# Performance work log

Hardware: AMD Instinct MI355X
Metric: run time of the kernel (lower is better)

The kernel has to match this reference:

```python
import jax, jax.numpy as jnp
import numpy as np

S, B, H = 512, 256, 500


def setup_inputs() -> dict:
    key = jax.random.key(0)
    k1, k2, k3, k4, k5 = jax.random.split(key, 5)
    return {
        "hidden": jax.random.normal(k1, (1, B, H), dtype=jnp.float32),
        "encoder_output": jax.random.normal(k2, (S, B, H), dtype=jnp.float32),
        "W_attn": jax.random.normal(k3, (H, 2 * H), dtype=jnp.float32) * 0.02,
        "b_attn": jax.random.normal(k4, (H,), dtype=jnp.float32) * 0.02,
        "v": jax.random.normal(k5, (H,), dtype=jnp.float32),
    }


def reference(hidden, encoder_output, W_attn, b_attn, v):
    # hidden: [1, B, H] -> broadcast to [S, B, H]; concat -> [S, B, 2H]
    s, b, h = encoder_output.shape
    h_exp = jnp.broadcast_to(hidden, (s, b, h))
    cat = jnp.concatenate([h_exp, encoder_output], axis=2)  # [S, B, 2H]
    # Linear(2H -> H) with torch convention W: [out, in], then tanh
    energy = jnp.tanh(jnp.einsum("sbi,hi->sbh", cat, W_attn) + b_attn)  # [S, B, H]
    scores = jnp.einsum("sbh,h->sb", energy, v)  # [S, B]
    attn = jax.nn.softmax(scores.T, axis=1)  # [B, S]
    return attn[:, None, :]  # [B, 1, S]
```

## Files before the change

kernel.cpp:

```cpp
#include <hip/hip_runtime.h>
#include <hip/hip_fp16.h>

#define S_DIM 512
#define B_DIM 256
#define H_DIM 500
#define HP    512
#define M_DIM (S_DIM * B_DIM)

typedef _Float16 half8_t __attribute__((ext_vector_type(8)));
typedef float    f32x4  __attribute__((ext_vector_type(4)));

#define WS_W2H 0
#define WS_A   (512 * 1024)
#define WS_VP  (1024 * 1024)
#define WS_SC  (1024 * 1024 + 4096)

__global__ void prep_w2_v(const float* __restrict__ W, const float* __restrict__ v,
                          _Float16* __restrict__ W2h, float* __restrict__ vp) {
    int idx = blockIdx.x * blockDim.x + threadIdx.x;
#pragma unroll
    for (int r = 0; r < 2; ++r) {
        int e = idx + r * 131072;
        int h = e >> 9, k = e & 511;
        float val = (h < H_DIM && k < H_DIM) ? W[h * 1000 + 500 + k] : 0.0f;
        W2h[e] = (_Float16)val;
    }
    if (idx < HP) vp[idx] = (idx < H_DIM) ? v[idx] : 0.0f;
}

__global__ void prep_A(const float* __restrict__ hidden, const float* __restrict__ W,
                       const float* __restrict__ b_attn, float* __restrict__ A) {
    int b = blockIdx.x;
    int t = threadIdx.x;
    __shared__ float hs[HP];
    hs[t] = (t < H_DIM) ? hidden[b * H_DIM + t] : 0.0f;
    __syncthreads();
    float acc = 0.0f;
    if (t < H_DIM) {
        acc = b_attn[t];
        const float4* wr = (const float4*)(W + t * 1000);
        const float4* hr = (const float4*)hs;
#pragma unroll 5
        for (int i = 0; i < 125; ++i) {
            float4 w4 = wr[i], h4 = hr[i];
            acc += w4.x * h4.x + w4.y * h4.y + w4.z * h4.z + w4.w * h4.w;
        }
    }
    A[b * HP + t] = acc;
}

__launch_bounds__(512, 2)
__global__ void fused_attn_gemm(const float* __restrict__ enc,
                                const _Float16* __restrict__ W2h,
                                const float* __restrict__ Aws,
                                const float* __restrict__ vp,
                                float* __restrict__ scores_t) {
    __shared__ _Float16 As[2][128][32];
    __shared__ _Float16 Bs[2][HP][32];
    __shared__ float    red[4][128];

    const int tid  = threadIdx.x;
    const int lane = tid & 63;
    const int wid  = tid >> 6;
    const int wm   = wid >> 2;
    const int wn   = wid & 3;
    const int l15  = lane & 15;
    const int lq   = lane >> 4;
    const int m0   = blockIdx.x * 128;

    const int srow = tid >> 2;
    const int sc0  = (tid & 3) * 8;

    f32x4 acc[4][8];
#pragma unroll
    for (int a = 0; a < 4; ++a)
#pragma unroll
        for (int b = 0; b < 8; ++b) acc[a][b] = 0;

    auto stage = [&](int buf, int kk) {
        {
            const float* g = enc + (size_t)(m0 + srow) * H_DIM;
            half8_t hv;
            if (kk + sc0 + 8 <= H_DIM) {
                float4 f0 = *(const float4*)(g + kk + sc0);
                float4 f1 = *(const float4*)(g + kk + sc0 + 4);
                hv[0] = (_Float16)f0.x; hv[1] = (_Float16)f0.y;
                hv[2] = (_Float16)f0.z; hv[3] = (_Float16)f0.w;
                hv[4] = (_Float16)f1.x; hv[5] = (_Float16)f1.y;
                hv[6] = (_Float16)f1.z; hv[7] = (_Float16)f1.w;
            } else {
#pragma unroll
                for (int u = 0; u < 8; ++u) {
                    int k = kk + sc0 + u;
                    hv[u] = (k < H_DIM) ? (_Float16)g[k] : (_Float16)0.0f;
                }
            }
            *(half8_t*)&As[buf][srow][sc0] = hv;
        }
#pragma unroll
        for (int r = 0; r < 4; ++r) {
            int row = srow + r * 128;
            half8_t hv = *(const half8_t*)(W2h + row * HP + kk + sc0);
            *(half8_t*)&Bs[buf][row][sc0] = hv;
        }
    };

    stage(0, 0);
#pragma unroll 2
    for (int ks = 0; ks < 16; ++ks) {
        int cur = ks & 1;
        __syncthreads();
        if (ks + 1 < 16) stage(cur ^ 1, (ks + 1) * 32);

        half8_t af[4], bf[8];
#pragma unroll
        for (int mf = 0; mf < 4; ++mf)
            af[mf] = *(const half8_t*)&As[cur][wm * 64 + mf * 16 + l15][lq * 8];
#pragma unroll
        for (int nf = 0; nf < 8; ++nf)
            bf[nf] = *(const half8_t*)&Bs[cur][wn * 128 + nf * 16 + l15][lq * 8];
#pragma unroll
        for (int mf = 0; mf < 4; ++mf)
#pragma unroll
            for (int nf = 0; nf < 8; ++nf)
                acc[mf][nf] = __builtin_amdgcn_mfma_f32_16x16x32_f16(af[mf], bf[nf], acc[mf][nf], 0, 0, 0);
    }

    float vpv[8];
#pragma unroll
    for (int nf = 0; nf < 8; ++nf) vpv[nf] = vp[wn * 128 + nf * 16 + l15];

    const int bloc  = (blockIdx.x & 1) * 128 + wm * 64;
    const int s_idx = blockIdx.x >> 1;

#pragma unroll
    for (int mf = 0; mf < 4; ++mf) {
        float pj[4] = {0, 0, 0, 0};
#pragma unroll
        for (int nf = 0; nf < 8; ++nf) {
            int h = wn * 128 + nf * 16 + l15;
#pragma unroll
            for (int j = 0; j < 4; ++j) {
                int b = bloc + mf * 16 + lq * 4 + j;
                float x = acc[mf][nf][j] + Aws[b * HP + h];
                float xc = fminf(fmaxf(x, -9.0f), 9.0f);
                float e  = __expf(2.0f * xc);
                float th = (e - 1.0f) / (e + 1.0f);
                pj[j] += vpv[nf] * th;
            }
        }
#pragma unroll
        for (int j = 0; j < 4; ++j) {
            float s = pj[j];
            s += __shfl_xor(s, 1); s += __shfl_xor(s, 2);
            s += __shfl_xor(s, 4); s += __shfl_xor(s, 8);
            if (l15 == 0) red[wn][wm * 64 + mf * 16 + lq * 4 + j] = s;
        }
    }
    __syncthreads();
    if (tid < 128) {
        float sc = red[0][tid] + red[1][tid] + red[2][tid] + red[3][tid];
        int b = (blockIdx.x & 1) * 128 + tid;
        scores_t[b * S_DIM + s_idx] = sc;
    }
}

__global__ void softmax_rows(const float* __restrict__ scores_t, float* __restrict__ out) {
    int b = blockIdx.x;
    int t = threadIdx.x;
    int lane = t & 63, wid = t >> 6;
    float v0 = scores_t[b * S_DIM + t];
    float v1 = scores_t[b * S_DIM + t + 256];
    float m = fmaxf(v0, v1);
#pragma unroll
    for (int off = 1; off < 64; off <<= 1) m = fmaxf(m, __shfl_xor(m, off));
    __shared__ float sm[4], ss[4];
    if (lane == 0) sm[wid] = m;
    __syncthreads();
    m = fmaxf(fmaxf(sm[0], sm[1]), fmaxf(sm[2], sm[3]));
    float e0 = __expf(v0 - m), e1 = __expf(v1 - m);
    float sum = e0 + e1;
#pragma unroll
    for (int off = 1; off < 64; off <<= 1) sum += __shfl_xor(sum, off);
    if (lane == 0) ss[wid] = sum;
    __syncthreads();
    sum = ss[0] + ss[1] + ss[2] + ss[3];
    float inv = 1.0f / sum;
    out[b * S_DIM + t]       = e0 * inv;
    out[b * S_DIM + t + 256] = e1 * inv;
}

extern "C" void kernel_launch(void* const* d_in, const int* in_sizes, int n_in,
                              void* d_out, int out_size, void* d_ws, size_t ws_size,
                              hipStream_t stream) {
    const float* hidden = (const float*)d_in[0];
    const float* enc    = (const float*)d_in[1];
    const float* W      = (const float*)d_in[2];
    const float* b_attn = (const float*)d_in[3];
    const float* v      = (const float*)d_in[4];
    float* out = (float*)d_out;

    char* ws = (char*)d_ws;
    _Float16* W2h = (_Float16*)(ws + WS_W2H);
    float*    A   = (float*)(ws + WS_A);
    float*    vp  = (float*)(ws + WS_VP);
    float*    sct = (float*)(ws + WS_SC);

    prep_w2_v<<<512, 256, 0, stream>>>(W, v, W2h, vp);
    prep_A<<<256, 512, 0, stream>>>(hidden, W, b_attn, A);
    fused_attn_gemm<<<1024, 512, 0, stream>>>(enc, W2h, A, vp, sct);
    softmax_rows<<<256, 256, 0, stream>>>(sct, out);
}
```

Baseline: 198.3 us.

## Split GEMM over N into four blocks with async B loads and swizzled LDS

Tiles the fused GEMM over both M and N (128x128 per block, 256 threads) instead of covering all of H per block. Partial score sums are written per N-block and reduced in the softmax kernel. B tiles are loaded directly into LDS with global_load_lds, and LDS columns are XOR-swizzled to avoid bank conflicts. The encoder global loads are issued before the MFMAs and converted afterwards to overlap latency. The trade-off is that the fp32 encoder tile is re-read and re-converted by four blocks, in exchange for higher occupancy and lower register use.

```diff
diff --git a/kernel.cpp b/kernel.cpp
--- a/kernel.cpp
+++ b/kernel.cpp
@@ -14,6 +14,12 @@
 #define WS_A   (512 * 1024)
 #define WS_VP  (1024 * 1024)
 #define WS_SC  (1024 * 1024 + 4096)
+
+__device__ __forceinline__ void gld_lds16(const void* g, void* l) {
+    __builtin_amdgcn_global_load_lds(
+        (const __attribute__((address_space(1))) unsigned int*)g,
+        (__attribute__((address_space(3))) unsigned int*)l, 16, 0, 0);
+}
 
 __global__ void prep_w2_v(const float* __restrict__ W, const float* __restrict__ v,
                           _Float16* __restrict__ W2h, float* __restrict__ vp) {
@@ -49,99 +55,127 @@
     A[b * HP + t] = acc;
 }
 
-__launch_bounds__(512, 2)
+__launch_bounds__(256, 4)
 __global__ void fused_attn_gemm(const float* __restrict__ enc,
                                 const _Float16* __restrict__ W2h,
                                 const float* __restrict__ Aws,
                                 const float* __restrict__ vp,
-                                float* __restrict__ scores_t) {
+                                float* __restrict__ sct) {
     __shared__ _Float16 As[2][128][32];
-    __shared__ _Float16 Bs[2][HP][32];
-    __shared__ float    red[4][128];
+    __shared__ _Float16 Bs[2][128][32];
+    __shared__ float    red[2][128];
 
     const int tid  = threadIdx.x;
     const int lane = tid & 63;
     const int wid  = tid >> 6;
-    const int wm   = wid >> 2;
-    const int wn   = wid & 3;
+    const int wm   = wid >> 1;
+    const int wn   = wid & 1;
     const int l15  = lane & 15;
     const int lq   = lane >> 4;
-    const int m0   = blockIdx.x * 128;
-
-    const int srow = tid >> 2;
-    const int sc0  = (tid & 3) * 8;
-
-    f32x4 acc[4][8];
+
+    const int mblk = blockIdx.x >> 2;
+    const int nblk = blockIdx.x & 3;
+    const int m0   = mblk * 128;
+    const int n0   = nblk * 128;
+
+    const int r0 = tid >> 2;
+    const int r1 = r0 + 64;
+    const int c  = tid & 3;
+
+    const float* gA0 = enc + (size_t)(m0 + r0) * H_DIM + c * 8;
+    const float* gA1 = enc + (size_t)(m0 + r1) * H_DIM + c * 8;
+    const int ca0 = (c ^ (r0 & 3)) * 8;
+    const int ca1 = (c ^ (r1 & 3)) * 8;
+
+    const int brow0 = (wid * 64 + lane) >> 2;
+    const int brow1 = brow0 + 64;
+    const _Float16* gB0 = W2h + (size_t)(n0 + brow0) * HP + ((c ^ (brow0 & 3)) * 8);
+    const _Float16* gB1 = W2h + (size_t)(n0 + brow1) * HP + ((c ^ (brow1 & 3)) * 8);
+
+    f32x4 acc[4][4];
 #pragma unroll
     for (int a = 0; a < 4; ++a)
 #pragma unroll
-        for (int b = 0; b < 8; ++b) acc[a][b] = 0;
-
-    auto stage = [&](int buf, int kk) {
-        {
-            const float* g = enc + (size_t)(m0 + srow) * H_DIM;
-            half8_t hv;
-            if (kk + sc0 + 8 <= H_DIM) {
-                float4 f0 = *(const float4*)(g + kk + sc0);
-                float4 f1 = *(const float4*)(g + kk + sc0 + 4);
-                hv[0] = (_Float16)f0.x; hv[1] = (_Float16)f0.y;
-                hv[2] = (_Float16)f0.z; hv[3] = (_Float16)f0.w;
-                hv[4] = (_Float16)f1.x; hv[5] = (_Float16)f1.y;
-                hv[6] = (_Float16)f1.z; hv[7] = (_Float16)f1.w;
-            } else {
-#pragma unroll
-                for (int u = 0; u < 8; ++u) {
-                    int k = kk + sc0 + u;
-                    hv[u] = (k < H_DIM) ? (_Float16)g[k] : (_Float16)0.0f;
-                }
+        for (int b = 0; b < 4; ++b) acc[a][b] = 0;
+
+    f32x4 ax0, ax1, ay0, ay1;
+
+    auto ldA = [&](int kk) {
+        if (kk < 480) {
+            ax0 = *(const f32x4*)(gA0 + kk); ax1 = *(const f32x4*)(gA0 + kk + 4);
+            ay0 = *(const f32x4*)(gA1 + kk); ay1 = *(const f32x4*)(gA1 + kk + 4);
+        } else {
+#pragma unroll
+            for (int u = 0; u < 4; ++u) {
+                int k = kk + c * 8 + u;
+                ax0[u] = (k < H_DIM) ? gA0[kk + u] : 0.0f;
+                ay0[u] = (k < H_DIM) ? gA1[kk + u] : 0.0f;
+                int k2 = k + 4;
+                ax1[u] = (k2 < H_DIM) ? gA0[kk + 4 + u] : 0.0f;
+                ay1[u] = (k2 < H_DIM) ? gA1[kk + 4 + u] : 0.0f;
             }
-            *(half8_t*)&As[buf][srow][sc0] = hv;
-        }
-#pragma unroll
-        for (int r = 0; r < 4; ++r) {
-            int row = srow + r * 128;
-            half8_t hv = *(const half8_t*)(W2h + row * HP + kk + sc0);
-            *(half8_t*)&Bs[buf][row][sc0] = hv;
         }
     };
-
-    stage(0, 0);
-#pragma unroll 2
+    auto wrA = [&](int buf) {
+        half8_t h0, h1;
+#pragma unroll
+        for (int u = 0; u < 4; ++u) {
+            h0[u] = (_Float16)ax0[u]; h0[u + 4] = (_Float16)ax1[u];
+            h1[u] = (_Float16)ay0[u]; h1[u + 4] = (_Float16)ay1[u];
+        }
+        *(half8_t*)&As[buf][r0][ca0] = h0;
+        *(half8_t*)&As[buf][r1][ca1] = h1;
+    };
+    auto stB = [&](int buf, int kk) {
+        gld_lds16(gB0 + kk, &Bs[buf][wid * 16][0]);
+        gld_lds16(gB1 + kk, &Bs[buf][64 + wid * 16][0]);
+    };
+
+    ldA(0);
+    stB(0, 0);
+    wrA(0);
+
+    const int sc = (lq ^ (l15 & 3)) * 8;
+
     for (int ks = 0; ks < 16; ++ks) {
-        int cur = ks & 1;
+        const int  cur = ks & 1;
+        const bool nxt = (ks + 1 < 16);
         __syncthreads();
-        if (ks + 1 < 16) stage(cur ^ 1, (ks + 1) * 32);
-
-        half8_t af[4], bf[8];
+        if (nxt) {
+            stB(cur ^ 1, (ks + 1) * 32);
+            ldA((ks + 1) * 32);
+        }
+        half8_t af[4], bf[4];
 #pragma unroll
         for (int mf = 0; mf < 4; ++mf)
-            af[mf] = *(const half8_t*)&As[cur][wm * 64 + mf * 16 + l15][lq * 8];
-#pragma unroll
-        for (int nf = 0; nf < 8; ++nf)
-            bf[nf] = *(const half8_t*)&Bs[cur][wn * 128 + nf * 16 + l15][lq * 8];
+            af[mf] = *(const half8_t*)&As[cur][wm * 64 + mf * 16 + l15][sc];
+#pragma unroll
+        for (int nf = 0; nf < 4; ++nf)
+            bf[nf] = *(const half8_t*)&Bs[cur][wn * 64 + nf * 16 + l15][sc];
 #pragma unroll
         for (int mf = 0; mf < 4; ++mf)
 #pragma unroll
-            for (int nf = 0; nf < 8; ++nf)
+            for (int nf = 0; nf < 4; ++nf)
                 acc[mf][nf] = __builtin_amdgcn_mfma_f32_16x16x32_f16(af[mf], bf[nf], acc[mf][nf], 0, 0, 0);
-    }
-
-    float vpv[8];
-#pragma unroll
-    for (int nf = 0; nf < 8; ++nf) vpv[nf] = vp[wn * 128 + nf * 16 + l15];
-
-    const int bloc  = (blockIdx.x & 1) * 128 + wm * 64;
-    const int s_idx = blockIdx.x >> 1;
+        if (nxt) wrA(cur ^ 1);
+    }
+
+    float vpv[4];
+#pragma unroll
+    for (int nf = 0; nf < 4; ++nf) vpv[nf] = vp[n0 + wn * 64 + nf * 16 + l15];
+
+    const int s_idx = m0 >> 8;
+    const int bloc  = (mblk & 1) * 128;
 
 #pragma unroll
     for (int mf = 0; mf < 4; ++mf) {
         float pj[4] = {0, 0, 0, 0};
 #pragma unroll
-        for (int nf = 0; nf < 8; ++nf) {
-            int h = wn * 128 + nf * 16 + l15;
+        for (int nf = 0; nf < 4; ++nf) {
+            int h = n0 + wn * 64 + nf * 16 + l15;
 #pragma unroll
             for (int j = 0; j < 4; ++j) {
-                int b = bloc + mf * 16 + lq * 4 + j;
+                int b = bloc + wm * 64 + mf * 16 + lq * 4 + j;
                 float x = acc[mf][nf][j] + Aws[b * HP + h];
                 float xc = fminf(fmaxf(x, -9.0f), 9.0f);
                 float e  = __expf(2.0f * xc);
@@ -159,35 +193,36 @@
     }
     __syncthreads();
     if (tid < 128) {
-        float sc = red[0][tid] + red[1][tid] + red[2][tid] + red[3][tid];
-        int b = (blockIdx.x & 1) * 128 + tid;
-        scores_t[b * S_DIM + s_idx] = sc;
-    }
-}
-
-__global__ void softmax_rows(const float* __restrict__ scores_t, float* __restrict__ out) {
+        float p = red[0][tid] + red[1][tid];
+        sct[nblk * M_DIM + (bloc + tid) * S_DIM + s_idx] = p;
+    }
+}
+
+__global__ void softmax_rows(const float* __restrict__ sct, float* __restrict__ out) {
     int b = blockIdx.x;
     int t = threadIdx.x;
-    int lane = t & 63, wid = t >> 6;
-    float v0 = scores_t[b * S_DIM + t];
-    float v1 = scores_t[b * S_DIM + t + 256];
-    float m = fmaxf(v0, v1);
+    int lane = t & 63, w = t >> 6;
+    size_t idx = (size_t)b * S_DIM + t;
+    float v = sct[idx] + sct[idx + M_DIM] + sct[idx + 2 * M_DIM] + sct[idx + 3 * M_DIM];
+    float m = v;
 #pragma unroll
     for (int off = 1; off < 64; off <<= 1) m = fmaxf(m, __shfl_xor(m, off));
-    __shared__ float sm[4], ss[4];
-    if (lane == 0) sm[wid] = m;
-    __syncthreads();
-    m = fmaxf(fmaxf(sm[0], sm[1]), fmaxf(sm[2], sm[3]));
-    float e0 = __expf(v0 - m), e1 = __expf(v1 - m);
-    float sum = e0 + e1;
-#pragma unroll
-    for (int off = 1; off < 64; off <<= 1) sum += __shfl_xor(sum, off);
-    if (lane == 0) ss[wid] = sum;
-    __syncthreads();
-    sum = ss[0] + ss[1] + ss[2] + ss[3];
-    float inv = 1.0f / sum;
-    out[b * S_DIM + t]       = e0 * inv;
-    out[b * S_DIM + t + 256] = e1 * inv;
+    __shared__ float sm[8], ss[8];
+    if (lane == 0) sm[w] = m;
+    __syncthreads();
+    m = sm[0];
+#pragma unroll
+    for (int i = 1; i < 8; ++i) m = fmaxf(m, sm[i]);
+    float e = __expf(v - m);
+    float s = e;
+#pragma unroll
+    for (int off = 1; off < 64; off <<= 1) s += __shfl_xor(s, off);
+    if (lane == 0) ss[w] = s;
+    __syncthreads();
+    s = ss[0];
+#pragma unroll
+    for (int i = 1; i < 8; ++i) s += ss[i];
+    out[(size_t)b * S_DIM + t] = e / s;
 }
 
 extern "C" void kernel_launch(void* const* d_in, const int* in_sizes, int n_in,
@@ -208,6 +243,6 @@
 
     prep_w2_v<<<512, 256, 0, stream>>>(W, v, W2h, vp);
     prep_A<<<256, 512, 0, stream>>>(hidden, W, b_attn, A);
-    fused_attn_gemm<<<1024, 512, 0, stream>>>(enc, W2h, A, vp, sct);
-    softmax_rows<<<256, 256, 0, stream>>>(sct, out);
-}
+    fused_attn_gemm<<<4096, 256, 0, stream>>>(enc, W2h, A, vp, sct);
+    softmax_rows<<<256, 512, 0, stream>>>(sct, out);
+}
```

Result: slower. 272.2 us (+37.3%).
